# Kernel tuning notes

Measured on AMD Instinct MI355X. Metric: run time of the kernel, lower is better.

## Reference

```python
import jax, jax.numpy as jnp
import numpy as np

N_NODES = 100000
N_EDGES = 1600000
IN_DIM = 160
HID = 128
BN_EPS = 1e-5


def setup_inputs() -> dict:
    key = jax.random.key(0)
    ks = jax.random.split(key, 16)
    d = {}
    d['x'] = jax.random.normal(ks[0], (N_NODES, IN_DIM), dtype=jnp.float32)
    d['edge_index'] = jax.random.randint(ks[1], (2, N_EDGES), 0, N_NODES, dtype=jnp.int64)
    dims = [(IN_DIM, HID), (HID, HID), (HID, HID)]
    for i, (fi, fo) in enumerate(dims):
        s = 1.0 / np.sqrt(fi)
        d[f'wl{i}'] = jax.random.normal(ks[2 + 4 * i], (fi, fo), dtype=jnp.float32) * s
        d[f'wr{i}'] = jax.random.normal(ks[3 + 4 * i], (fi, fo), dtype=jnp.float32) * s
        d[f'bl{i}'] = jnp.zeros((fo,), dtype=jnp.float32)
        d[f'g{i}'] = jnp.ones((fo,), dtype=jnp.float32)
        d[f'be{i}'] = jnp.zeros((fo,), dtype=jnp.float32)
        d[f'rm{i}'] = jax.random.normal(ks[4 + 4 * i], (fo,), dtype=jnp.float32) * 0.1
        d[f'rv{i}'] = jnp.ones((fo,), dtype=jnp.float32)
    d['lin_w'] = jax.random.normal(ks[14], (HID, 1), dtype=jnp.float32) * (1.0 / np.sqrt(HID))
    d['lin_b'] = jnp.zeros((1,), dtype=jnp.float32)
    return d


def _sage_bn_relu(h, src, dst, wl, wr, bl, g, be, rm, rv):
    # mean neighbor aggregation: gather messages at src, scatter-mean to dst
    msg = h[src]                                            # [E, d]
    agg = jax.ops.segment_sum(msg, dst, num_segments=N_NODES)
    cnt = jax.ops.segment_sum(jnp.ones((msg.shape[0],), h.dtype), dst, num_segments=N_NODES)
    mean = agg / jnp.maximum(cnt, 1.0)[:, None]             # nodes w/o in-edges -> 0
    out = mean @ wl + bl + h @ wr                           # SAGEConv (root_weight=True)
    # BatchNorm1d (inference: running stats) + ReLU
    out = (out - rm) * (g * jax.lax.rsqrt(rv + BN_EPS)) + be
    return jax.nn.relu(out)


def reference(x, edge_index,
              wl0, wr0, bl0, g0, be0, rm0, rv0,
              wl1, wr1, bl1, g1, be1, rm1, rv1,
              wl2, wr2, bl2, g2, be2, rm2, rv2,
              lin_w, lin_b):
    src, dst = edge_index[0], edge_index[1]
    h = _sage_bn_relu(x, src, dst, wl0, wr0, bl0, g0, be0, rm0, rv0)
    h = _sage_bn_relu(h, src, dst, wl1, wr1, bl1, g1, be1, rm1, rv1)
    h = _sage_bn_relu(h, src, dst, wl2, wr2, bl2, g2, be2, rm2, rv2)
    return (h @ lin_w + lin_b)[:, 0]                        # [N]
```

## Files before the change

kernel.cpp:

```cpp
#include <hip/hip_runtime.h>

#define N_NODES 100000
#define N_EDGES 1600000
#define IN_DIM 160
#define HID 128
#define BN_EPS 1e-5f

#define M_PAD 100096
#define NBUCK 196
#define BSH 9
#define EPB 8192
#define NHB (NBUCK * NBUCK)
#define NSB 38
#define LPAD 132

typedef unsigned int uint;
typedef unsigned short ushort;
typedef __attribute__((ext_vector_type(8))) short bf16x8;
typedef __attribute__((ext_vector_type(4))) float f32x4;

__device__ __forceinline__ ushort bf16rn(float f) {
    uint u = __float_as_uint(f);
    u += 0x7fffu + ((u >> 16) & 1u);
    return (ushort)(u >> 16);
}
__device__ __forceinline__ float bflo(uint u) { return __uint_as_float(u << 16); }
__device__ __forceinline__ float bfhi(uint u) { return __uint_as_float(u & 0xffff0000u); }


__global__ __launch_bounds__(256) void hist_kernel(const int* __restrict__ dst,
                                                   int* __restrict__ ghist) {
    __shared__ int hist[NBUCK];
    int b = blockIdx.x, t = threadIdx.x;
    for (int i = t; i < NBUCK; i += 256) hist[i] = 0;
    __syncthreads();
    int e0 = b * EPB;
    for (int i = 0; i < EPB; i += 256) {
        int e = e0 + i + t;
        if (e < N_EDGES) atomicAdd(&hist[dst[e] >> BSH], 1);
    }
    __syncthreads();
    for (int i = t; i < NBUCK; i += 256) ghist[i * NBUCK + b] = hist[i];
}

__global__ __launch_bounds__(256) void scan1_kernel(const int* __restrict__ ghist,
                                                    int* __restrict__ bsum) {
    __shared__ int wsum[4];
    int b = blockIdx.x, t = threadIdx.x;
    int i4 = b * 256 + t;
    int4 v = (i4 * 4 < NHB) ? ((const int4*)ghist)[i4] : make_int4(0, 0, 0, 0);
    int s = v.x + v.y + v.z + v.w;
#pragma unroll
    for (int off = 32; off; off >>= 1) s += __shfl_down(s, off);
    if ((t & 63) == 0) wsum[t >> 6] = s;
    __syncthreads();
    if (t == 0) bsum[b] = wsum[0] + wsum[1] + wsum[2] + wsum[3];
}

__global__ void scan2_kernel(const int* __restrict__ bsum, int* __restrict__ boff,
                             int* __restrict__ gbb) {
    int lane = threadIdx.x;
    int v = (lane < NSB) ? bsum[lane] : 0;
    int s = v;
#pragma unroll
    for (int off = 1; off <= 32; off <<= 1) {
        int t2 = __shfl_up(s, off);
        if (lane >= off) s += t2;
    }
    if (lane < NSB) boff[lane] = s - v;
    if (lane == 0) gbb[NBUCK] = N_EDGES;
}

__global__ __launch_bounds__(256) void scan3_kernel(int* __restrict__ ghist,
                                                    const int* __restrict__ boff,
                                                    int* __restrict__ gbb) {
    __shared__ int ts[256];
    int b = blockIdx.x, t = threadIdx.x;
    int i4 = b * 256 + t;
    bool ok = (i4 * 4) < NHB;
    int4 v = ok ? ((const int4*)ghist)[i4] : make_int4(0, 0, 0, 0);
    int s = v.x + v.y + v.z + v.w;
    ts[t] = s;
    __syncthreads();
    for (int off = 1; off < 256; off <<= 1) {
        int a = (t >= off) ? ts[t - off] : 0;
        __syncthreads();
        ts[t] += a;
        __syncthreads();
    }
    int excl = boff[b] + ((t > 0) ? ts[t - 1] : 0);
    if (ok) {
        int idx = i4 * 4;
        int4 w;
        w.x = excl;
        w.y = excl + v.x;
        w.z = excl + v.x + v.y;
        w.w = excl + v.x + v.y + v.z;
        ((int4*)ghist)[i4] = w;
        if (idx % NBUCK == 0) gbb[idx / NBUCK] = w.x;
    }
}

__global__ __launch_bounds__(256) void scatter_kernel(const int* __restrict__ src,
                                                      const int* __restrict__ dst,
                                                      const int* __restrict__ ghist,
                                                      uint* __restrict__ scat) {
    __shared__ int base[NBUCK];
    __shared__ int fill[NBUCK];
    int b = blockIdx.x, t = threadIdx.x;
    for (int i = t; i < NBUCK; i += 256) { base[i] = ghist[i * NBUCK + b]; fill[i] = 0; }
    __syncthreads();
    int e0 = b * EPB;
    for (int i = 0; i < EPB; i += 256) {
        int e = e0 + i + t;
        if (e < N_EDGES) {
            int d = dst[e];
            int sv = src[e];
            int bk = d >> BSH;
            int lp = atomicAdd(&fill[bk], 1);
            scat[base[bk] + lp] = (uint)sv | ((uint)(d & 511) << 17);
        }
    }
}

__global__ __launch_bounds__(256) void bucket_csr_kernel(const uint* __restrict__ scat,
                                                         const int* __restrict__ gbb,
                                                         int* __restrict__ prow,
                                                         int* __restrict__ deg,
                                                         int* __restrict__ peidx) {
    __shared__ int cnt[512], fl[512], pref[512];
    __shared__ int ts[256];
    __shared__ int tot_s;
    int b = blockIdx.x, t = threadIdx.x;
    int beg = gbb[b], end = gbb[b + 1];
    int pb = beg + b * 8192;
    cnt[t] = 0; cnt[t + 256] = 0;
    __syncthreads();
    for (int i = beg + t; i < end; i += 256)
        atomicAdd(&cnt[scat[i] >> 17], 1);
    __syncthreads();
    int c0 = cnt[2 * t], c1 = cnt[2 * t + 1];
    int p0 = (c0 + 15) & ~15, p1 = (c1 + 15) & ~15;
    ts[t] = p0 + p1;
    __syncthreads();
    for (int off = 1; off < 256; off <<= 1) {
        int v = (t >= off) ? ts[t - off] : 0;
        __syncthreads();
        ts[t] += v;
        __syncthreads();
    }
    int ex = (t > 0) ? ts[t - 1] : 0;
    pref[2 * t] = ex;
    pref[2 * t + 1] = ex + p0;
    fl[t] = 0; fl[t + 256] = 0;
    if (t == 255) tot_s = ts[255];
    int g0 = b * 512 + 2 * t;
    if (g0 < N_NODES) { prow[g0] = pb + ex; deg[g0] = c0; }
    if (g0 + 1 < N_NODES) { prow[g0 + 1] = pb + ex + p0; deg[g0 + 1] = c1; }
    __syncthreads();
    int tot = tot_s;
    for (int i = t; i < tot; i += 256) peidx[pb + i] = 0;
    __syncthreads();
    for (int i = beg + t; i < end; i += 256) {
        uint w = scat[i];
        int nl = (int)(w >> 17);
        int lp = atomicAdd(&fl[nl], 1);
        peidx[pb + pref[nl] + lp] = (int)(w & 0x1FFFFu);
    }
}

__global__ void prep_weights_kernel(const float* __restrict__ wl, const float* __restrict__ wr,
                                    ushort* __restrict__ Bt, int K) {
    int n = blockIdx.y;
    int k = blockIdx.x * 64 + threadIdx.x;
    if (k < K) {
        float v = (n < HID) ? wl[k * HID + n] : wr[k * HID + (n - HID)];
        Bt[n * K + k] = bf16rn(v);
    }
}

__global__ void bn_prep_kernel(const float* __restrict__ bl, const float* __restrict__ g,
                               const float* __restrict__ be, const float* __restrict__ rm,
                               const float* __restrict__ rv, float* __restrict__ scale,
                               float* __restrict__ shift) {
    int j = threadIdx.x;
    float s = g[j] * rsqrtf(rv[j] + BN_EPS);
    scale[j] = s;
    shift[j] = (bl[j] - rm[j]) * s + be[j];
}

template <int K, bool AFP32>
__global__ __launch_bounds__(256) void gemm_kernel(const void* __restrict__ A_,
                                                   const ushort* __restrict__ Bt,
                                                   ushort* __restrict__ tl,
                                                   ushort* __restrict__ troot) {
    __shared__ ushort lds[4][16][LPAD];
    const int lane = threadIdx.x & 63;
    const int wv = threadIdx.x >> 6;
    const int col = lane & 15;
    const int kq = (lane >> 4) * 8;
    const int m0 = blockIdx.x * 128 + wv * 32 + col;
    const int nc0 = blockIdx.y * 128;
    ushort* outp = blockIdx.y ? troot : tl;
    f32x4 acc[2][8];
#pragma unroll
    for (int a = 0; a < 2; ++a)
#pragma unroll
        for (int t = 0; t < 8; ++t) acc[a][t] = (f32x4){0.f, 0.f, 0.f, 0.f};

#pragma unroll
    for (int k0 = 0; k0 < K; k0 += 32) {
        int kk = k0 + kq;
        bf16x8 a0, a1;
        if (AFP32) {
            const float* A = (const float*)A_;
            float4 z = make_float4(0.f, 0.f, 0.f, 0.f);
            float4 f00 = z, f01 = z, f10 = z, f11 = z;
            if (m0 < N_NODES) {
                f00 = *(const float4*)(A + (size_t)m0 * K + kk);
                f01 = *(const float4*)(A + (size_t)m0 * K + kk + 4);
            }
            if (m0 + 16 < N_NODES) {
                f10 = *(const float4*)(A + (size_t)(m0 + 16) * K + kk);
                f11 = *(const float4*)(A + (size_t)(m0 + 16) * K + kk + 4);
            }
            a0[0] = (short)bf16rn(f00.x); a0[1] = (short)bf16rn(f00.y);
            a0[2] = (short)bf16rn(f00.z); a0[3] = (short)bf16rn(f00.w);
            a0[4] = (short)bf16rn(f01.x); a0[5] = (short)bf16rn(f01.y);
            a0[6] = (short)bf16rn(f01.z); a0[7] = (short)bf16rn(f01.w);
            a1[0] = (short)bf16rn(f10.x); a1[1] = (short)bf16rn(f10.y);
            a1[2] = (short)bf16rn(f10.z); a1[3] = (short)bf16rn(f10.w);
            a1[4] = (short)bf16rn(f11.x); a1[5] = (short)bf16rn(f11.y);
            a1[6] = (short)bf16rn(f11.z); a1[7] = (short)bf16rn(f11.w);
        } else {
            const ushort* A = (const ushort*)A_;
            a0 = *(const bf16x8*)(A + (size_t)m0 * K + kk);
            a1 = *(const bf16x8*)(A + (size_t)(m0 + 16) * K + kk);
        }
#pragma unroll
        for (int t = 0; t < 8; ++t) {
            bf16x8 bfr = *(const bf16x8*)(Bt + (size_t)(nc0 + t * 16 + col) * K + kk);
            acc[0][t] = __builtin_amdgcn_mfma_f32_16x16x32_bf16(a0, bfr, acc[0][t], 0, 0, 0);
            acc[1][t] = __builtin_amdgcn_mfma_f32_16x16x32_bf16(a1, bfr, acc[1][t], 0, 0, 0);
        }
    }

    const int quad = lane >> 4;
#pragma unroll
    for (int mt = 0; mt < 2; ++mt) {
#pragma unroll
        for (int tt = 0; tt < 8; ++tt)
#pragma unroll
            for (int r = 0; r < 4; ++r)
                lds[wv][quad * 4 + r][tt * 16 + col] = bf16rn(acc[mt][tt][r]);
        int mbase = blockIdx.x * 128 + wv * 32 + mt * 16;
#pragma unroll
        for (int i = 0; i < 4; ++i) {
            int lin = i * 64 + lane;
            int row = lin >> 4;
            int c16 = lin & 15;
            bf16x8 v = *(const bf16x8*)&lds[wv][row][c16 * 8];
            *(bf16x8*)(outp + (size_t)(mbase + row) * HID + c16 * 8) = v;
        }
    }
}

template <bool FINAL>
__global__ __launch_bounds__(256) void agg_kernel(
    const ushort* __restrict__ tl_, const ushort* __restrict__ troot_,
    const int* __restrict__ prow, const int* __restrict__ deg_,
    const int* __restrict__ peidx,
    const float* __restrict__ bnscale, const float* __restrict__ bnshift,
    const float* __restrict__ linw, const float* __restrict__ linb,
    ushort* __restrict__ hout, float* __restrict__ out) {
    const int lane = threadIdx.x & 63;
    const int wvg = (blockIdx.x * 256 + (int)threadIdx.x) >> 6;
    const int g = lane >> 4;
    const int s = lane & 15;
    const int n = wvg * 4 + g;
    const int nn = (n < N_NODES) ? n : (N_NODES - 1);

    float4 sc0 = *(const float4*)(bnscale + s * 8);
    float4 sc1 = *(const float4*)(bnscale + s * 8 + 4);
    float4 sh0 = *(const float4*)(bnshift + s * 8);
    float4 sh1 = *(const float4*)(bnshift + s * 8 + 4);

    int pbeg = prow[nn];
    int dg = (n < N_NODES) ? deg_[nn] : 0;
    int myb = (dg + 15) >> 4;

    float acc[8];
#pragma unroll
    for (int i = 0; i < 8; ++i) acc[i] = 0.f;

    const int gsel = (lane & 48) << 2;

    for (int b = 0;; ++b) {
        bool act = b < myb;
        if (!__any(act)) break;
        int base = act ? (pbeg + b * 16) : 0;
        int idx = peidx[base + s];
#pragma unroll
        for (int jj = 0; jj < 16; ++jj) {
            int src = __builtin_amdgcn_ds_bpermute(gsel | (jj << 2), idx);
            bool val = (b * 16 + jj) < dg;
            src = val ? src : 0;
            uint4 v = *(const uint4*)(tl_ + (size_t)src * HID + s * 8);
            float m = val ? 1.f : 0.f;
            acc[0] = fmaf(m, bflo(v.x), acc[0]);
            acc[1] = fmaf(m, bfhi(v.x), acc[1]);
            acc[2] = fmaf(m, bflo(v.y), acc[2]);
            acc[3] = fmaf(m, bfhi(v.y), acc[3]);
            acc[4] = fmaf(m, bflo(v.z), acc[4]);
            acc[5] = fmaf(m, bfhi(v.z), acc[5]);
            acc[6] = fmaf(m, bflo(v.w), acc[6]);
            acc[7] = fmaf(m, bfhi(v.w), acc[7]);
        }
    }

    float inv = 1.0f / (float)((dg > 0) ? dg : 1);
    uint4 rv = *(const uint4*)(troot_ + (size_t)nn * HID + s * 8);
    float o[8];
    o[0] = fmaxf(fmaf(fmaf(acc[0], inv, bflo(rv.x)), sc0.x, sh0.x), 0.f);
    o[1] = fmaxf(fmaf(fmaf(acc[1], inv, bfhi(rv.x)), sc0.y, sh0.y), 0.f);
    o[2] = fmaxf(fmaf(fmaf(acc[2], inv, bflo(rv.y)), sc0.z, sh0.z), 0.f);
    o[3] = fmaxf(fmaf(fmaf(acc[3], inv, bfhi(rv.y)), sc0.w, sh0.w), 0.f);
    o[4] = fmaxf(fmaf(fmaf(acc[4], inv, bflo(rv.z)), sc1.x, sh1.x), 0.f);
    o[5] = fmaxf(fmaf(fmaf(acc[5], inv, bfhi(rv.z)), sc1.y, sh1.y), 0.f);
    o[6] = fmaxf(fmaf(fmaf(acc[6], inv, bflo(rv.w)), sc1.z, sh1.z), 0.f);
    o[7] = fmaxf(fmaf(fmaf(acc[7], inv, bfhi(rv.w)), sc1.w, sh1.w), 0.f);

    if (FINAL) {
        float4 w0 = *(const float4*)(linw + s * 8);
        float4 w1 = *(const float4*)(linw + s * 8 + 4);
        float p = o[0] * w0.x + o[1] * w0.y + o[2] * w0.z + o[3] * w0.w +
                  o[4] * w1.x + o[5] * w1.y + o[6] * w1.z + o[7] * w1.w;
#pragma unroll
        for (int off = 1; off < 16; off <<= 1) p += __shfl_xor(p, off);
        if (s == 0 && n < N_NODES) out[n] = p + linb[0];
    } else {
        uint4 pk;
        pk.x = (uint)bf16rn(o[0]) | ((uint)bf16rn(o[1]) << 16);
        pk.y = (uint)bf16rn(o[2]) | ((uint)bf16rn(o[3]) << 16);
        pk.z = (uint)bf16rn(o[4]) | ((uint)bf16rn(o[5]) << 16);
        pk.w = (uint)bf16rn(o[6]) | ((uint)bf16rn(o[7]) << 16);
        if (n < N_NODES) *(uint4*)(hout + (size_t)n * HID + s * 8) = pk;
    }
}


extern "C" void kernel_launch(void* const* d_in, const int* in_sizes, int n_in,
                              void* d_out, int out_size, void* d_ws, size_t ws_size,
                              hipStream_t stream) {
    const float* x    = (const float*)d_in[0];
    const int*   ei   = (const int*)d_in[1];
    const int*   esrc = ei;
    const int*   edst = ei + N_EDGES;
    const float* wl[3]; const float* wr[3]; const float* bl[3];
    const float* g[3];  const float* be[3]; const float* rm[3]; const float* rv[3];
    for (int i = 0; i < 3; ++i) {
        wl[i] = (const float*)d_in[2 + 7 * i];
        wr[i] = (const float*)d_in[3 + 7 * i];
        bl[i] = (const float*)d_in[4 + 7 * i];
        g[i]  = (const float*)d_in[5 + 7 * i];
        be[i] = (const float*)d_in[6 + 7 * i];
        rm[i] = (const float*)d_in[7 + 7 * i];
        rv[i] = (const float*)d_in[8 + 7 * i];
    }
    const float* lin_w = (const float*)d_in[23];
    const float* lin_b = (const float*)d_in[24];
    float* out = (float*)d_out;

    char* ws = (char*)d_ws;
    size_t off = 0;
    auto carve = [&](size_t bytes) -> void* {
        void* p = ws + off;
        off += (bytes + 255) & ~(size_t)255;
        return p;
    };
    int*    prow   = (int*)carve((size_t)(N_NODES + 8) * sizeof(int));
    int*    deg    = (int*)carve((size_t)(N_NODES + 8) * sizeof(int));
    int*    peidx  = (int*)carve((size_t)3210000 * sizeof(int));
    uint*   scat   = (uint*)carve((size_t)N_EDGES * sizeof(uint));
    int*    ghist  = (int*)carve((size_t)(NSB * 1024) * sizeof(int));
    int*    gbb    = (int*)carve((NBUCK + 4) * sizeof(int));
    int*    bsum   = (int*)carve((NSB + 2) * sizeof(int));
    int*    boff   = (int*)carve((NSB + 2) * sizeof(int));
    ushort* tl     = (ushort*)carve((size_t)M_PAD * HID * sizeof(ushort));
    ushort* troot  = (ushort*)carve((size_t)M_PAD * HID * sizeof(ushort));
    ushort* h      = (ushort*)carve((size_t)M_PAD * HID * sizeof(ushort));
    ushort* Bt0    = (ushort*)carve(256 * IN_DIM * sizeof(ushort));
    ushort* Bt1    = (ushort*)carve(256 * HID * sizeof(ushort));
    ushort* Bt2    = (ushort*)carve(256 * HID * sizeof(ushort));
    float*  bnsc   = (float*)carve(3 * HID * sizeof(float));
    float*  bnsh   = (float*)carve(3 * HID * sizeof(float));
    (void)ws_size; (void)n_in; (void)in_sizes; (void)out_size;

    hist_kernel<<<NBUCK, 256, 0, stream>>>(edst, ghist);
    scan1_kernel<<<NSB, 256, 0, stream>>>(ghist, bsum);
    scan2_kernel<<<1, 64, 0, stream>>>(bsum, boff, gbb);
    scan3_kernel<<<NSB, 256, 0, stream>>>(ghist, boff, gbb);
    scatter_kernel<<<NBUCK, 256, 0, stream>>>(esrc, edst, ghist, scat);
    bucket_csr_kernel<<<NBUCK, 256, 0, stream>>>(scat, gbb, prow, deg, peidx);

    prep_weights_kernel<<<dim3((IN_DIM + 63) / 64, 256), 64, 0, stream>>>(wl[0], wr[0], Bt0, IN_DIM);
    prep_weights_kernel<<<dim3((HID + 63) / 64, 256), 64, 0, stream>>>(wl[1], wr[1], Bt1, HID);
    prep_weights_kernel<<<dim3((HID + 63) / 64, 256), 64, 0, stream>>>(wl[2], wr[2], Bt2, HID);
    bn_prep_kernel<<<1, HID, 0, stream>>>(bl[0], g[0], be[0], rm[0], rv[0], bnsc, bnsh);
    bn_prep_kernel<<<1, HID, 0, stream>>>(bl[1], g[1], be[1], rm[1], rv[1], bnsc + HID, bnsh + HID);
    bn_prep_kernel<<<1, HID, 0, stream>>>(bl[2], g[2], be[2], rm[2], rv[2], bnsc + 2 * HID, bnsh + 2 * HID);

    const dim3 GEMM_GRID(M_PAD / 128, 2);
    const int AGG_GRID = (N_NODES + 15) / 16;

    gemm_kernel<IN_DIM, true><<<GEMM_GRID, 256, 0, stream>>>(x, Bt0, tl, troot);
    agg_kernel<false><<<AGG_GRID, 256, 0, stream>>>(tl, troot, prow, deg, peidx, bnsc, bnsh,
                                                    nullptr, nullptr, h, nullptr);
    gemm_kernel<HID, false><<<GEMM_GRID, 256, 0, stream>>>(h, Bt1, tl, troot);
    agg_kernel<false><<<AGG_GRID, 256, 0, stream>>>(tl, troot, prow, deg, peidx, bnsc + HID, bnsh + HID,
                                                    nullptr, nullptr, h, nullptr);
    gemm_kernel<HID, false><<<GEMM_GRID, 256, 0, stream>>>(h, Bt2, tl, troot);
    agg_kernel<true><<<AGG_GRID, 256, 0, stream>>>(tl, troot, prow, deg, peidx, bnsc + 2 * HID, bnsh + 2 * HID,
                                                   lin_w, lin_b, nullptr, out);
}
```

Before: 507.6 us.

## Stage GEMM A tile in swizzled LDS, batch gather loads in aggregation, merge BN prep

The GEMM now loads the full 128-row A tile into LDS once, converting to bf16 and using an XOR swizzle, then reads MFMA fragments from LDS. This avoids each wave fetching and converting A from global memory on its own. The aggregation kernel issues all 16 neighbour-row loads before accumulating, so more memory requests are in flight, and it adds a launch-bounds occupancy hint. The three BN prep launches are merged into one. The larger LDS use (up to 40KB) and the 16 uint4 registers per thread may lower occupancy.

```diff
diff --git a/kernel.cpp b/kernel.cpp
--- a/kernel.cpp
+++ b/kernel.cpp
@@ -179,14 +179,26 @@
     }
 }
 
-__global__ void bn_prep_kernel(const float* __restrict__ bl, const float* __restrict__ g,
-                               const float* __restrict__ be, const float* __restrict__ rm,
-                               const float* __restrict__ rv, float* __restrict__ scale,
-                               float* __restrict__ shift) {
-    int j = threadIdx.x;
+__global__ void bn_prep_kernel(const float* __restrict__ bl0, const float* __restrict__ g0,
+                               const float* __restrict__ be0, const float* __restrict__ rm0,
+                               const float* __restrict__ rv0,
+                               const float* __restrict__ bl1, const float* __restrict__ g1,
+                               const float* __restrict__ be1, const float* __restrict__ rm1,
+                               const float* __restrict__ rv1,
+                               const float* __restrict__ bl2, const float* __restrict__ g2,
+                               const float* __restrict__ be2, const float* __restrict__ rm2,
+                               const float* __restrict__ rv2,
+                               float* __restrict__ scale, float* __restrict__ shift) {
+    int t = threadIdx.x;
+    int L = t >> 7, j = t & 127;
+    const float* bl = (L == 0) ? bl0 : (L == 1) ? bl1 : bl2;
+    const float* g  = (L == 0) ? g0  : (L == 1) ? g1  : g2;
+    const float* be = (L == 0) ? be0 : (L == 1) ? be1 : be2;
+    const float* rm = (L == 0) ? rm0 : (L == 1) ? rm1 : rm2;
+    const float* rv = (L == 0) ? rv0 : (L == 1) ? rv1 : rv2;
     float s = g[j] * rsqrtf(rv[j] + BN_EPS);
-    scale[j] = s;
-    shift[j] = (bl[j] - rm[j]) * s + be[j];
+    scale[t] = s;
+    shift[t] = (bl[j] - rm[j]) * s + be[j];
 }
 
 template <int K, bool AFP32>
@@ -194,79 +206,92 @@
                                                    const ushort* __restrict__ Bt,
                                                    ushort* __restrict__ tl,
                                                    ushort* __restrict__ troot) {
-    __shared__ ushort lds[4][16][LPAD];
+    constexpr int CPR = (K * 2) / 16;
+    constexpr int FULLG = CPR & ~7;
+    __shared__ ushort ldsA[128 * K];
+    const int t = threadIdx.x;
+    const int m0b = blockIdx.x * 128;
+
+#pragma unroll
+    for (int i = 0; i < (128 * CPR) / 256; ++i) {
+        int cidx = i * 256 + t;
+        int row = cidx / CPR;
+        int j = cidx - row * CPR;
+        bf16x8 v;
+        if (AFP32) {
+            const float* A = (const float*)A_;
+            int m = m0b + row;
+            float4 f0 = make_float4(0.f, 0.f, 0.f, 0.f), f1 = f0;
+            if (m < N_NODES) {
+                f0 = *(const float4*)(A + (size_t)m * K + j * 8);
+                f1 = *(const float4*)(A + (size_t)m * K + j * 8 + 4);
+            }
+            v[0] = (short)bf16rn(f0.x); v[1] = (short)bf16rn(f0.y);
+            v[2] = (short)bf16rn(f0.z); v[3] = (short)bf16rn(f0.w);
+            v[4] = (short)bf16rn(f1.x); v[5] = (short)bf16rn(f1.y);
+            v[6] = (short)bf16rn(f1.z); v[7] = (short)bf16rn(f1.w);
+        } else {
+            const ushort* A = (const ushort*)A_;
+            v = *(const bf16x8*)(A + (size_t)(m0b + row) * K + j * 8);
+        }
+        int swz = (j < FULLG) ? ((j & ~7) | ((j ^ row) & 7))
+                              : ((j & ~3) | ((j ^ row) & 3));
+        *(bf16x8*)&ldsA[row * K + swz * 8] = v;
+    }
+    __syncthreads();
+
     const int lane = threadIdx.x & 63;
     const int wv = threadIdx.x >> 6;
     const int col = lane & 15;
-    const int kq = (lane >> 4) * 8;
-    const int m0 = blockIdx.x * 128 + wv * 32 + col;
+    const int q = lane >> 4;
     const int nc0 = blockIdx.y * 128;
+    const int row0 = wv * 32 + col;
+    f32x4 acc[2][8];
+#pragma unroll
+    for (int a = 0; a < 2; ++a)
+#pragma unroll
+        for (int tt = 0; tt < 8; ++tt) acc[a][tt] = (f32x4){0.f, 0.f, 0.f, 0.f};
+
+#pragma unroll
+    for (int k0 = 0; k0 < K; k0 += 32) {
+        int jj = (k0 >> 3) + q;
+        int swzj = (jj < FULLG) ? ((jj & ~7) | ((jj ^ col) & 7))
+                                : ((jj & ~3) | ((jj ^ col) & 3));
+        bf16x8 a0 = *(const bf16x8*)&ldsA[row0 * K + swzj * 8];
+        bf16x8 a1 = *(const bf16x8*)&ldsA[(row0 + 16) * K + swzj * 8];
+        int kk = k0 + q * 8;
+#pragma unroll
+        for (int tt = 0; tt < 8; ++tt) {
+            bf16x8 bfr = *(const bf16x8*)(Bt + (size_t)(nc0 + tt * 16 + col) * K + kk);
+            acc[0][tt] = __builtin_amdgcn_mfma_f32_16x16x32_bf16(a0, bfr, acc[0][tt], 0, 0, 0);
+            acc[1][tt] = __builtin_amdgcn_mfma_f32_16x16x32_bf16(a1, bfr, acc[1][tt], 0, 0, 0);
+        }
+    }
+
+    __syncthreads();
+    ushort(*rp)[16][LPAD] = (ushort(*)[16][LPAD])ldsA;
     ushort* outp = blockIdx.y ? troot : tl;
-    f32x4 acc[2][8];
-#pragma unroll
-    for (int a = 0; a < 2; ++a)
-#pragma unroll
-        for (int t = 0; t < 8; ++t) acc[a][t] = (f32x4){0.f, 0.f, 0.f, 0.f};
-
-#pragma unroll
-    for (int k0 = 0; k0 < K; k0 += 32) {
-        int kk = k0 + kq;
-        bf16x8 a0, a1;
-        if (AFP32) {
-            const float* A = (const float*)A_;
-            float4 z = make_float4(0.f, 0.f, 0.f, 0.f);
-            float4 f00 = z, f01 = z, f10 = z, f11 = z;
-            if (m0 < N_NODES) {
-                f00 = *(const float4*)(A + (size_t)m0 * K + kk);
-                f01 = *(const float4*)(A + (size_t)m0 * K + kk + 4);
-            }
-            if (m0 + 16 < N_NODES) {
-                f10 = *(const float4*)(A + (size_t)(m0 + 16) * K + kk);
-                f11 = *(const float4*)(A + (size_t)(m0 + 16) * K + kk + 4);
-            }
-            a0[0] = (short)bf16rn(f00.x); a0[1] = (short)bf16rn(f00.y);
-            a0[2] = (short)bf16rn(f00.z); a0[3] = (short)bf16rn(f00.w);
-            a0[4] = (short)bf16rn(f01.x); a0[5] = (short)bf16rn(f01.y);
-            a0[6] = (short)bf16rn(f01.z); a0[7] = (short)bf16rn(f01.w);
-            a1[0] = (short)bf16rn(f10.x); a1[1] = (short)bf16rn(f10.y);
-            a1[2] = (short)bf16rn(f10.z); a1[3] = (short)bf16rn(f10.w);
-            a1[4] = (short)bf16rn(f11.x); a1[5] = (short)bf16rn(f11.y);
-            a1[6] = (short)bf16rn(f11.z); a1[7] = (short)bf16rn(f11.w);
-        } else {
-            const ushort* A = (const ushort*)A_;
-            a0 = *(const bf16x8*)(A + (size_t)m0 * K + kk);
-            a1 = *(const bf16x8*)(A + (size_t)(m0 + 16) * K + kk);
-        }
-#pragma unroll
-        for (int t = 0; t < 8; ++t) {
-            bf16x8 bfr = *(const bf16x8*)(Bt + (size_t)(nc0 + t * 16 + col) * K + kk);
-            acc[0][t] = __builtin_amdgcn_mfma_f32_16x16x32_bf16(a0, bfr, acc[0][t], 0, 0, 0);
-            acc[1][t] = __builtin_amdgcn_mfma_f32_16x16x32_bf16(a1, bfr, acc[1][t], 0, 0, 0);
-        }
-    }
-
-    const int quad = lane >> 4;
 #pragma unroll
     for (int mt = 0; mt < 2; ++mt) {
 #pragma unroll
         for (int tt = 0; tt < 8; ++tt)
 #pragma unroll
             for (int r = 0; r < 4; ++r)
-                lds[wv][quad * 4 + r][tt * 16 + col] = bf16rn(acc[mt][tt][r]);
+                rp[wv][q * 4 + r][tt * 16 + col] = bf16rn(acc[mt][tt][r]);
         int mbase = blockIdx.x * 128 + wv * 32 + mt * 16;
 #pragma unroll
         for (int i = 0; i < 4; ++i) {
             int lin = i * 64 + lane;
             int row = lin >> 4;
             int c16 = lin & 15;
-            bf16x8 v = *(const bf16x8*)&lds[wv][row][c16 * 8];
+            bf16x8 v = *(const bf16x8*)&rp[wv][row][c16 * 8];
             *(bf16x8*)(outp + (size_t)(mbase + row) * HID + c16 * 8) = v;
         }
     }
 }
 
 template <bool FINAL>
-__global__ __launch_bounds__(256) void agg_kernel(
+__global__ __launch_bounds__(256, 2) void agg_kernel(
     const ushort* __restrict__ tl_, const ushort* __restrict__ troot_,
     const int* __restrict__ prow, const int* __restrict__ deg_,
     const int* __restrict__ peidx,
@@ -300,21 +325,24 @@
         if (!__any(act)) break;
         int base = act ? (pbeg + b * 16) : 0;
         int idx = peidx[base + s];
+        uint4 u[16];
 #pragma unroll
         for (int jj = 0; jj < 16; ++jj) {
             int src = __builtin_amdgcn_ds_bpermute(gsel | (jj << 2), idx);
-            bool val = (b * 16 + jj) < dg;
-            src = val ? src : 0;
-            uint4 v = *(const uint4*)(tl_ + (size_t)src * HID + s * 8);
-            float m = val ? 1.f : 0.f;
-            acc[0] = fmaf(m, bflo(v.x), acc[0]);
-            acc[1] = fmaf(m, bfhi(v.x), acc[1]);
-            acc[2] = fmaf(m, bflo(v.y), acc[2]);
-            acc[3] = fmaf(m, bfhi(v.y), acc[3]);
-            acc[4] = fmaf(m, bflo(v.z), acc[4]);
-            acc[5] = fmaf(m, bfhi(v.z), acc[5]);
-            acc[6] = fmaf(m, bflo(v.w), acc[6]);
-            acc[7] = fmaf(m, bfhi(v.w), acc[7]);
+            src = ((b * 16 + jj) < dg) ? src : 0;
+            u[jj] = *(const uint4*)(tl_ + (size_t)src * HID + s * 8);
+        }
+#pragma unroll
+        for (int jj = 0; jj < 16; ++jj) {
+            float m = ((b * 16 + jj) < dg) ? 1.f : 0.f;
+            acc[0] = fmaf(m, bflo(u[jj].x), acc[0]);
+            acc[1] = fmaf(m, bfhi(u[jj].x), acc[1]);
+            acc[2] = fmaf(m, bflo(u[jj].y), acc[2]);
+            acc[3] = fmaf(m, bfhi(u[jj].y), acc[3]);
+            acc[4] = fmaf(m, bflo(u[jj].z), acc[4]);
+            acc[5] = fmaf(m, bfhi(u[jj].z), acc[5]);
+            acc[6] = fmaf(m, bflo(u[jj].w), acc[6]);
+            acc[7] = fmaf(m, bfhi(u[jj].w), acc[7]);
         }
     }
 
@@ -406,9 +434,10 @@
     prep_weights_kernel<<<dim3((IN_DIM + 63) / 64, 256), 64, 0, stream>>>(wl[0], wr[0], Bt0, IN_DIM);
     prep_weights_kernel<<<dim3((HID + 63) / 64, 256), 64, 0, stream>>>(wl[1], wr[1], Bt1, HID);
     prep_weights_kernel<<<dim3((HID + 63) / 64, 256), 64, 0, stream>>>(wl[2], wr[2], Bt2, HID);
-    bn_prep_kernel<<<1, HID, 0, stream>>>(bl[0], g[0], be[0], rm[0], rv[0], bnsc, bnsh);
-    bn_prep_kernel<<<1, HID, 0, stream>>>(bl[1], g[1], be[1], rm[1], rv[1], bnsc + HID, bnsh + HID);
-    bn_prep_kernel<<<1, HID, 0, stream>>>(bl[2], g[2], be[2], rm[2], rv[2], bnsc + 2 * HID, bnsh + 2 * HID);
+    bn_prep_kernel<<<1, 384, 0, stream>>>(bl[0], g[0], be[0], rm[0], rv[0],
+                                          bl[1], g[1], be[1], rm[1], rv[1],
+                                          bl[2], g[2], be[2], rm[2], rv[2],
+                                          bnsc, bnsh);
 
     const dim3 GEMM_GRID(M_PAD / 128, 2);
     const int AGG_GRID = (N_NODES + 15) / 16;
```

Measured after the change: 514.6 us. No clear change (+1.4%).
